# Kernel optimization log

Hardware: AMD Instinct MI355X
Metric: run time of the kernel (lower is better)

## Reference

```python
import jax, jax.numpy as jnp
import numpy as np

N_INNER, N_OUTER = 384, 192  # log-spaced samples as in render()
N_RAYS = 1024
EPS = 1e-10

def _z_vals():
    # torch.logspace is base-10, matching jnp.logspace
    return jnp.concatenate([jnp.logspace(-1.2, 0.0, N_INNER),
                            jnp.logspace(0.0, 2.0, N_OUTER)]).astype(jnp.float32)  # [N]

def _z_lin():
    z = jnp.concatenate([jnp.linspace(-1.2, 0.0, N_INNER),
                         jnp.linspace(0.0, 2.0, N_OUTER)]).astype(jnp.float32)
    return (z + 1.2) / 3.2  # normalized to [0,1], [N]

def _render_rays(sigmas, rgbs, z_vals):
    # Standard alpha compositing (reconstruction of helpers.render_rays_log_new)
    deltas = jnp.diff(z_vals)                                   # [N-1]
    deltas = jnp.concatenate([deltas, jnp.full((1,), 1e10, deltas.dtype)])  # [N]
    alpha = 1.0 - jnp.exp(-sigmas * deltas[None, :])            # [R,N]
    # exclusive cumulative transmittance
    trans = jnp.cumprod(1.0 - alpha + EPS, axis=1)
    trans = jnp.concatenate([jnp.ones_like(trans[:, :1]), trans[:, :-1]], axis=1)
    weights = alpha * trans                                     # [R,N]
    image = jnp.einsum('rn,rnc->rc', weights, rgbs)             # [R,3]
    invdepth = jnp.sum(weights / z_vals[None, :], axis=1)       # [R]
    return image, invdepth, weights

def setup_inputs() -> dict:
    key = jax.random.key(0)
    k1, k2 = jax.random.split(key)
    sigmas = jax.random.uniform(k1, (N_RAYS, N_INNER + N_OUTER), dtype=jnp.float32)
    rgbs = jax.random.uniform(k2, (N_RAYS, N_INNER + N_OUTER, 3), dtype=jnp.float32)
    return {"sigmas": sigmas, "rgbs": rgbs}

def reference(sigmas, rgbs):
    z_vals = _z_vals()
    image, invdepth, weights = _render_rays(sigmas, rgbs, z_vals)
    # distortion loss: sum_ij w_i w_j |t_i - t_j| per ray.
    # Original does bmm(w[:,:,None], w[:,None,:]) * |ti-tj| then sum -> O(R*N^2) memory.
    # Identical math via w^T S w: (weights @ S) then row-dot, no [R,N,N] tensor.
    z_lin = _z_lin()
    S = jnp.abs(z_lin[:, None] - z_lin[None, :])                # [N,N]
    l_per_ray = jnp.sum(weights * (weights @ S), axis=1)        # [R]
    l_dist = jnp.mean(l_per_ray)
    return image[None, ...], invdepth[None, ...], l_dist
```

## Files before the change

### kernel.cpp

```cpp
#include <hip/hip_runtime.h>


#define NSAMP 576
#define NRAYS 1024

__device__ __forceinline__ float zexp(int i) {
    if (i < 384) return -1.2f + (float)i * (1.2f / 383.0f);
    return (float)(i - 384) * (2.0f / 191.0f);
}
__device__ __forceinline__ float zval(int i) {
    const float LOG2_10 = 3.3219280948873623f;
    return exp2f(zexp(i) * LOG2_10);
}
__device__ __forceinline__ float tval(int i) {
    return (zexp(i) + 1.2f) * (1.0f / 3.2f);
}

__global__ __launch_bounds__(256) void render_kernel(
    const float* __restrict__ sigmas,
    const float* __restrict__ rgbs,
    float* __restrict__ out,
    float* __restrict__ wsum)
{
    const float LOG2_E = 1.4426950408889634f;
    const int lane = threadIdx.x & 63;
    const int ray  = blockIdx.x * 4 + (threadIdx.x >> 6);

    const float* __restrict__ sig = sigmas + (size_t)ray * NSAMP;
    const float* __restrict__ rgb = rgbs  + (size_t)ray * NSAMP * 3;

    float runP = 1.0f;
    float runW = 0.0f;
    float runT = 0.0f;
    float imR = 0.0f, imG = 0.0f, imB = 0.0f, invd = 0.0f, dist = 0.0f;

    #pragma unroll
    for (int k = 0; k < 9; ++k) {
        const int s = k * 64 + lane;
        const float sg = sig[s];
        const float r0 = rgb[s * 3 + 0];
        const float g0 = rgb[s * 3 + 1];
        const float b0 = rgb[s * 3 + 2];

        const float z = zval(s);
        const float delta = (s == NSAMP - 1) ? 1e10f : (zval(s + 1) - z);
        const float t = tval(s);

        const float e  = exp2f(-sg * delta * LOG2_E);
        const float alpha = 1.0f - e;
        const float om = e + 1e-10f;

        float p = om;
        #pragma unroll
        for (int off = 1; off < 64; off <<= 1) {
            float o = __shfl_up(p, off, 64);
            if (lane >= off) p *= o;
        }
        float exP = __shfl_up(p, 1, 64);
        if (lane == 0) exP = 1.0f;

        const float w  = alpha * (runP * exP);
        const float wt = w * t;

        float sw = w, swt = wt;
        #pragma unroll
        for (int off = 1; off < 64; off <<= 1) {
            float a = __shfl_up(sw,  off, 64);
            float b = __shfl_up(swt, off, 64);
            if (lane >= off) { sw += a; swt += b; }
        }
        const float exW  = sw  - w;
        const float exWT = swt - wt;

        dist += w * (t * (runW + exW) - (runT + exWT));
        imR  += w * r0;
        imG  += w * g0;
        imB  += w * b0;
        invd += w / z;

        runP *= __shfl(p,   63, 64);
        runW += __shfl(sw,  63, 64);
        runT += __shfl(swt, 63, 64);
    }

    #pragma unroll
    for (int off = 32; off; off >>= 1) {
        imR  += __shfl_down(imR,  off, 64);
        imG  += __shfl_down(imG,  off, 64);
        imB  += __shfl_down(imB,  off, 64);
        invd += __shfl_down(invd, off, 64);
        dist += __shfl_down(dist, off, 64);
    }

    if (lane == 0) {
        out[ray * 3 + 0] = imR;
        out[ray * 3 + 1] = imG;
        out[ray * 3 + 2] = imB;
        out[3 * NRAYS + ray] = invd;
        wsum[ray] = 2.0f * dist;
    }
}

__global__ __launch_bounds__(256) void reduce_kernel(
    const float* __restrict__ wsum, float* __restrict__ out)
{
    const int tid = threadIdx.x;
    float v = wsum[tid] + wsum[tid + 256] + wsum[tid + 512] + wsum[tid + 768];
    #pragma unroll
    for (int off = 32; off; off >>= 1) v += __shfl_down(v, off, 64);

    __shared__ float partial[4];
    if ((tid & 63) == 0) partial[tid >> 6] = v;
    __syncthreads();
    if (tid == 0)
        out[3 * NRAYS + NRAYS] =
            (partial[0] + partial[1] + partial[2] + partial[3]) * (1.0f / 1024.0f);
}

extern "C" void kernel_launch(void* const* d_in, const int* in_sizes, int n_in,
                              void* d_out, int out_size, void* d_ws, size_t ws_size,
                              hipStream_t stream) {
    const float* sigmas = (const float*)d_in[0];
    const float* rgbs   = (const float*)d_in[1];
    float* out = (float*)d_out;
    float* ws  = (float*)d_ws;

    render_kernel<<<NRAYS / 4, 256, 0, stream>>>(sigmas, rgbs, out, ws);
    reduce_kernel<<<1, 256, 0, stream>>>(ws, out);
}
```

Baseline: 12.22 us.

## Batch all chunk loads and interleave independent scans across chunks

The render kernel now issues all nine chunks' loads up front into registers. It then runs the wave-level prefix product and prefix-sum scans for all chunks at once, so the shuffle chains are independent and can interleave instead of serializing through a running carry. The divide by z is replaced with a precomputed reciprocal via exp2, and the final reduction kernel is shrunk to a single wavefront with no shared memory or barrier. This raises register pressure in exchange for more instruction-level parallelism and memory-level parallelism.

```diff
diff --git a/kernel.cpp b/kernel.cpp
--- a/kernel.cpp
+++ b/kernel.cpp
@@ -3,17 +3,11 @@
 
 #define NSAMP 576
 #define NRAYS 1024
+#define NCH 9
 
 __device__ __forceinline__ float zexp(int i) {
     if (i < 384) return -1.2f + (float)i * (1.2f / 383.0f);
     return (float)(i - 384) * (2.0f / 191.0f);
-}
-__device__ __forceinline__ float zval(int i) {
-    const float LOG2_10 = 3.3219280948873623f;
-    return exp2f(zexp(i) * LOG2_10);
-}
-__device__ __forceinline__ float tval(int i) {
-    return (zexp(i) + 1.2f) * (1.0f / 3.2f);
 }
 
 __global__ __launch_bounds__(256) void render_kernel(
@@ -22,65 +16,96 @@
     float* __restrict__ out,
     float* __restrict__ wsum)
 {
-    const float LOG2_E = 1.4426950408889634f;
+    const float L10 = 3.3219280948873623f;
+    const float LE  = 1.4426950408889634f;
     const int lane = threadIdx.x & 63;
     const int ray  = blockIdx.x * 4 + (threadIdx.x >> 6);
 
     const float* __restrict__ sig = sigmas + (size_t)ray * NSAMP;
     const float* __restrict__ rgb = rgbs  + (size_t)ray * NSAMP * 3;
 
-    float runP = 1.0f;
-    float runW = 0.0f;
-    float runT = 0.0f;
-    float imR = 0.0f, imG = 0.0f, imB = 0.0f, invd = 0.0f, dist = 0.0f;
+    float sg[NCH], r0[NCH], g0[NCH], b0[NCH];
+    #pragma unroll
+    for (int k = 0; k < NCH; ++k) {
+        const int s = k * 64 + lane;
+        sg[k] = sig[s];
+        r0[k] = rgb[s * 3 + 0];
+        g0[k] = rgb[s * 3 + 1];
+        b0[k] = rgb[s * 3 + 2];
+    }
+
+    float t[NCH], rz[NCH], p[NCH], al[NCH];
+    #pragma unroll
+    for (int k = 0; k < NCH; ++k) {
+        const int s = k * 64 + lane;
+        const float e0 = zexp(s);
+        const float z  = exp2f(e0 * L10);
+        rz[k] = exp2f(-e0 * L10);
+        t[k]  = (e0 + 1.2f) * (1.0f / 3.2f);
+        const float dlt = (s == NSAMP - 1) ? 1e10f : (exp2f(zexp(s + 1) * L10) - z);
+        const float e = exp2f(-sg[k] * dlt * LE);
+        al[k] = 1.0f - e;
+        p[k]  = e + 1e-10f;
+    }
 
     #pragma unroll
-    for (int k = 0; k < 9; ++k) {
-        const int s = k * 64 + lane;
-        const float sg = sig[s];
-        const float r0 = rgb[s * 3 + 0];
-        const float g0 = rgb[s * 3 + 1];
-        const float b0 = rgb[s * 3 + 2];
+    for (int off = 1; off < 64; off <<= 1) {
+        float sh[NCH];
+        #pragma unroll
+        for (int k = 0; k < NCH; ++k) sh[k] = __shfl_up(p[k], off, 64);
+        #pragma unroll
+        for (int k = 0; k < NCH; ++k) if (lane >= off) p[k] *= sh[k];
+    }
 
-        const float z = zval(s);
-        const float delta = (s == NSAMP - 1) ? 1e10f : (zval(s + 1) - z);
-        const float t = tval(s);
+    float tot[NCH], exP[NCH];
+    #pragma unroll
+    for (int k = 0; k < NCH; ++k) {
+        tot[k] = __shfl(p[k], 63, 64);
+        exP[k] = __shfl_up(p[k], 1, 64);
+        if (lane == 0) exP[k] = 1.0f;
+    }
+    float w[NCH];
+    {
+        float cP = 1.0f;
+        #pragma unroll
+        for (int k = 0; k < NCH; ++k) {
+            w[k] = al[k] * cP * exP[k];
+            cP *= tot[k];
+        }
+    }
 
-        const float e  = exp2f(-sg * delta * LOG2_E);
-        const float alpha = 1.0f - e;
-        const float om = e + 1e-10f;
+    float sw[NCH], st[NCH];
+    #pragma unroll
+    for (int k = 0; k < NCH; ++k) { sw[k] = w[k]; st[k] = w[k] * t[k]; }
+    #pragma unroll
+    for (int off = 1; off < 64; off <<= 1) {
+        float a[NCH], b[NCH];
+        #pragma unroll
+        for (int k = 0; k < NCH; ++k) {
+            a[k] = __shfl_up(sw[k], off, 64);
+            b[k] = __shfl_up(st[k], off, 64);
+        }
+        #pragma unroll
+        for (int k = 0; k < NCH; ++k)
+            if (lane >= off) { sw[k] += a[k]; st[k] += b[k]; }
+    }
 
-        float p = om;
+    float imR = 0.f, imG = 0.f, imB = 0.f, invd = 0.f, dist = 0.f;
+    {
+        float cW = 0.f, cT = 0.f;
         #pragma unroll
-        for (int off = 1; off < 64; off <<= 1) {
-            float o = __shfl_up(p, off, 64);
-            if (lane >= off) p *= o;
+        for (int k = 0; k < NCH; ++k) {
+            const float wk = w[k];
+            const float exW = cW + sw[k] - wk;
+            const float exT = cT + st[k] - wk * t[k];
+            dist += wk * (t[k] * exW - exT);
+            imR  += wk * r0[k];
+            imG  += wk * g0[k];
+            imB  += wk * b0[k];
+            invd += wk * rz[k];
+            cW += __shfl(sw[k], 63, 64);
+            cT += __shfl(st[k], 63, 64);
         }
-        float exP = __shfl_up(p, 1, 64);
-        if (lane == 0) exP = 1.0f;
-
-        const float w  = alpha * (runP * exP);
-        const float wt = w * t;
-
-        float sw = w, swt = wt;
-        #pragma unroll
-        for (int off = 1; off < 64; off <<= 1) {
-            float a = __shfl_up(sw,  off, 64);
-            float b = __shfl_up(swt, off, 64);
-            if (lane >= off) { sw += a; swt += b; }
-        }
-        const float exW  = sw  - w;
-        const float exWT = swt - wt;
-
-        dist += w * (t * (runW + exW) - (runT + exWT));
-        imR  += w * r0;
-        imG  += w * g0;
-        imB  += w * b0;
-        invd += w / z;
-
-        runP *= __shfl(p,   63, 64);
-        runW += __shfl(sw,  63, 64);
-        runT += __shfl(swt, 63, 64);
     }
 
     #pragma unroll
@@ -101,20 +126,16 @@
     }
 }
 
-__global__ __launch_bounds__(256) void reduce_kernel(
+__global__ __launch_bounds__(64) void reduce_kernel(
     const float* __restrict__ wsum, float* __restrict__ out)
 {
-    const int tid = threadIdx.x;
-    float v = wsum[tid] + wsum[tid + 256] + wsum[tid + 512] + wsum[tid + 768];
+    const int lane = threadIdx.x;
+    float v = 0.f;
+    #pragma unroll
+    for (int j = 0; j < 16; ++j) v += wsum[lane + 64 * j];
     #pragma unroll
     for (int off = 32; off; off >>= 1) v += __shfl_down(v, off, 64);
-
-    __shared__ float partial[4];
-    if ((tid & 63) == 0) partial[tid >> 6] = v;
-    __syncthreads();
-    if (tid == 0)
-        out[3 * NRAYS + NRAYS] =
-            (partial[0] + partial[1] + partial[2] + partial[3]) * (1.0f / 1024.0f);
+    if (lane == 0) out[3 * NRAYS + NRAYS] = v * (1.0f / 1024.0f);
 }
 
 extern "C" void kernel_launch(void* const* d_in, const int* in_sizes, int n_in,
@@ -126,5 +147,5 @@
     float* ws  = (float*)d_ws;
 
     render_kernel<<<NRAYS / 4, 256, 0, stream>>>(sigmas, rgbs, out, ws);
-    reduce_kernel<<<1, 256, 0, stream>>>(ws, out);
+    reduce_kernel<<<1, 64, 0, stream>>>(ws, out);
 }
```

After: 12.82 us. 1.05x slower.

## Stage ray data in LDS and use per-lane serial chunks with one wave scan

Applied to the files above, without the earlier changes.

Each wave loads its ray's sigmas and rgbs into shared memory with float4 loads. Each lane then owns 9 contiguous samples, so a single product scan and a single sum scan replace the nine per-iteration scans. The distortion term is rewritten with the total weight sum, which removes the weighted-time scan, and the reciprocal of z is computed directly with exp2. This cuts shuffle traffic and uses wider global loads, but adds LDS use (36KB per block), stride-9 and stride-27 LDS reads that may cause bank conflicts, and a block-wide sync. The reduce kernel is also shrunk to one wave using float4 loads.

```diff
diff --git a/kernel.cpp b/kernel.cpp
--- a/kernel.cpp
+++ b/kernel.cpp
@@ -3,17 +3,11 @@
 
 #define NSAMP 576
 #define NRAYS 1024
+#define RPB 4
 
 __device__ __forceinline__ float zexp(int i) {
     if (i < 384) return -1.2f + (float)i * (1.2f / 383.0f);
     return (float)(i - 384) * (2.0f / 191.0f);
-}
-__device__ __forceinline__ float zval(int i) {
-    const float LOG2_10 = 3.3219280948873623f;
-    return exp2f(zexp(i) * LOG2_10);
-}
-__device__ __forceinline__ float tval(int i) {
-    return (zexp(i) + 1.2f) * (1.0f / 3.2f);
 }
 
 __global__ __launch_bounds__(256) void render_kernel(
@@ -22,65 +16,96 @@
     float* __restrict__ out,
     float* __restrict__ wsum)
 {
-    const float LOG2_E = 1.4426950408889634f;
+    const float L10 = 3.3219280948873623f;
+    const float LE  = 1.4426950408889634f;
+    __shared__ float lds[RPB * 2304];
+
     const int lane = threadIdx.x & 63;
-    const int ray  = blockIdx.x * 4 + (threadIdx.x >> 6);
+    const int wid  = threadIdx.x >> 6;
+    const int ray  = blockIdx.x * RPB + wid;
+    float* my = lds + wid * 2304;
 
-    const float* __restrict__ sig = sigmas + (size_t)ray * NSAMP;
-    const float* __restrict__ rgb = rgbs  + (size_t)ray * NSAMP * 3;
+    const float4* sig4 = (const float4*)(sigmas + (size_t)ray * NSAMP);
+    const float4* rgb4 = (const float4*)(rgbs  + (size_t)ray * NSAMP * 3);
+    float4* ls = (float4*)my;
+    float4* lr = (float4*)(my + NSAMP);
 
-    float runP = 1.0f;
-    float runW = 0.0f;
-    float runT = 0.0f;
-    float imR = 0.0f, imG = 0.0f, imB = 0.0f, invd = 0.0f, dist = 0.0f;
+    float4 s0 = sig4[lane];
+    float4 s1 = sig4[64 + lane];
+    float4 s2; if (lane < 16) s2 = sig4[128 + lane];
+    float4 r0 = rgb4[lane],        r1 = rgb4[64 + lane],  r2 = rgb4[128 + lane];
+    float4 r3 = rgb4[192 + lane],  r4 = rgb4[256 + lane], r5 = rgb4[320 + lane];
+    float4 r6; if (lane < 48) r6 = rgb4[384 + lane];
 
+    ls[lane] = s0; ls[64 + lane] = s1; if (lane < 16) ls[128 + lane] = s2;
+    lr[lane] = r0; lr[64 + lane] = r1; lr[128 + lane] = r2;
+    lr[192 + lane] = r3; lr[256 + lane] = r4; lr[320 + lane] = r5;
+    if (lane < 48) lr[384 + lane] = r6;
+    __syncthreads();
+
+    const int sbase = lane * 9;
+    float z[10];
     #pragma unroll
-    for (int k = 0; k < 9; ++k) {
-        const int s = k * 64 + lane;
-        const float sg = sig[s];
-        const float r0 = rgb[s * 3 + 0];
-        const float g0 = rgb[s * 3 + 1];
-        const float b0 = rgb[s * 3 + 2];
+    for (int j = 0; j < 10; ++j) z[j] = exp2f(zexp(sbase + j) * L10);
 
-        const float z = zval(s);
-        const float delta = (s == NSAMP - 1) ? 1e10f : (zval(s + 1) - z);
-        const float t = tval(s);
+    float om[9], al[9], t[9], rz[9];
+    float Pin = 1.0f;
+    #pragma unroll
+    for (int j = 0; j < 9; ++j) {
+        const int s = sbase + j;
+        const float e0 = zexp(s);
+        t[j]  = (e0 + 1.2f) * (1.0f / 3.2f);
+        rz[j] = exp2f(-e0 * L10);
+        const float dlt = (s == NSAMP - 1) ? 1e10f : (z[j + 1] - z[j]);
+        const float sg = my[s - sbase + sbase];
+        const float e = exp2f(-my[s] * dlt * LE);
+        (void)sg;
+        al[j] = 1.0f - e;
+        om[j] = e + 1e-10f;
+        Pin *= om[j];
+    }
 
-        const float e  = exp2f(-sg * delta * LOG2_E);
-        const float alpha = 1.0f - e;
-        const float om = e + 1e-10f;
+    float inc = Pin;
+    #pragma unroll
+    for (int off = 1; off < 64; off <<= 1) {
+        float o = __shfl_up(inc, off, 64);
+        if (lane >= off) inc *= o;
+    }
+    float Tcar = __shfl_up(inc, 1, 64);
+    if (lane == 0) Tcar = 1.0f;
 
-        float p = om;
+    float w[9];
+    float swl = 0.f, imR = 0.f, imG = 0.f, imB = 0.f, invd = 0.f;
+    {
+        float cur = Tcar;
         #pragma unroll
-        for (int off = 1; off < 64; off <<= 1) {
-            float o = __shfl_up(p, off, 64);
-            if (lane >= off) p *= o;
+        for (int j = 0; j < 9; ++j) {
+            const int s = sbase + j;
+            const float wk = al[j] * cur;
+            cur *= om[j];
+            w[j] = wk;
+            swl += wk;
+            imR += wk * my[NSAMP + s * 3 + 0];
+            imG += wk * my[NSAMP + s * 3 + 1];
+            imB += wk * my[NSAMP + s * 3 + 2];
+            invd += wk * rz[j];
         }
-        float exP = __shfl_up(p, 1, 64);
-        if (lane == 0) exP = 1.0f;
+    }
 
-        const float w  = alpha * (runP * exP);
-        const float wt = w * t;
+    float incs = swl;
+    #pragma unroll
+    for (int off = 1; off < 64; off <<= 1) {
+        float a = __shfl_up(incs, off, 64);
+        if (lane >= off) incs += a;
+    }
+    const float Sw = __shfl(incs, 63, 64);
+    float runW = incs - swl;
 
-        float sw = w, swt = wt;
-        #pragma unroll
-        for (int off = 1; off < 64; off <<= 1) {
-            float a = __shfl_up(sw,  off, 64);
-            float b = __shfl_up(swt, off, 64);
-            if (lane >= off) { sw += a; swt += b; }
-        }
-        const float exW  = sw  - w;
-        const float exWT = swt - wt;
-
-        dist += w * (t * (runW + exW) - (runT + exWT));
-        imR  += w * r0;
-        imG  += w * g0;
-        imB  += w * b0;
-        invd += w / z;
-
-        runP *= __shfl(p,   63, 64);
-        runW += __shfl(sw,  63, 64);
-        runT += __shfl(swt, 63, 64);
+    float dist = 0.f;
+    #pragma unroll
+    for (int j = 0; j < 9; ++j) {
+        dist += w[j] * t[j] * (2.0f * runW + w[j] - Sw);
+        runW += w[j];
     }
 
     #pragma unroll
@@ -101,20 +126,17 @@
     }
 }
 
-__global__ __launch_bounds__(256) void reduce_kernel(
+__global__ __launch_bounds__(64) void reduce_kernel(
     const float* __restrict__ wsum, float* __restrict__ out)
 {
-    const int tid = threadIdx.x;
-    float v = wsum[tid] + wsum[tid + 256] + wsum[tid + 512] + wsum[tid + 768];
+    const int lane = threadIdx.x;
+    const float4* w4 = (const float4*)wsum;
+    float4 a = w4[lane], b = w4[64 + lane], c = w4[128 + lane], d = w4[192 + lane];
+    float v = (a.x + a.y + a.z + a.w) + (b.x + b.y + b.z + b.w)
+            + (c.x + c.y + c.z + c.w) + (d.x + d.y + d.z + d.w);
     #pragma unroll
     for (int off = 32; off; off >>= 1) v += __shfl_down(v, off, 64);
-
-    __shared__ float partial[4];
-    if ((tid & 63) == 0) partial[tid >> 6] = v;
-    __syncthreads();
-    if (tid == 0)
-        out[3 * NRAYS + NRAYS] =
-            (partial[0] + partial[1] + partial[2] + partial[3]) * (1.0f / 1024.0f);
+    if (lane == 0) out[3 * NRAYS + NRAYS] = v * (1.0f / 1024.0f);
 }
 
 extern "C" void kernel_launch(void* const* d_in, const int* in_sizes, int n_in,
@@ -125,6 +147,6 @@
     float* out = (float*)d_out;
     float* ws  = (float*)d_ws;
 
-    render_kernel<<<NRAYS / 4, 256, 0, stream>>>(sigmas, rgbs, out, ws);
-    reduce_kernel<<<1, 256, 0, stream>>>(ws, out);
+    render_kernel<<<NRAYS / RPB, 256, 0, stream>>>(sigmas, rgbs, out, ws);
+    reduce_kernel<<<1, 64, 0, stream>>>(ws, out);
 }
```

Measured after the change: 11.58 us. -5.2%, faster.
